# Optimization experiments

Measured on AMD Instinct MI355X. Metric: run time of the kernel, lower is better.

The kernel has to match this reference:

```python
import jax, jax.numpy as jnp
import numpy as np

B, T, N, D = 32, 50, 100, 4
E = N * (N - 1)
N_IN, N_HID, N_OUT = T * D, 256, 4


def _mlp(x, w1, b1, w2, b2):
    # Linear -> ReLU -> (dropout=0) -> Linear
    return jax.nn.relu(x @ w1 + b1) @ w2 + b2


def setup_inputs() -> dict:
    key = jax.random.key(0)
    ks = jax.random.split(key, 12)
    # fully-connected directed graph, no self loops
    idx = np.array([(i, j) for i in range(N) for j in range(N) if i != j], dtype=np.int64)
    recv, sendr = idx[:, 0], idx[:, 1]
    rec = jnp.asarray(np.eye(N, dtype=np.float32)[recv])    # [E, N]
    send = jnp.asarray(np.eye(N, dtype=np.float32)[sendr])  # [E, N]

    def lin(k, fan_in, fan_out):
        kw, kb = jax.random.split(k)
        w = jax.random.normal(kw, (fan_in, fan_out), jnp.float32) * 0.02
        b = jax.random.normal(kb, (fan_out,), jnp.float32) * 0.02
        return w, b

    x = jax.random.normal(ks[0], (B, T, N, D), jnp.float32)
    w1a, b1a = lin(ks[1], N_IN, N_HID)
    w1b, b1b = lin(ks[2], N_HID, N_HID)
    w2a, b2a = lin(ks[3], 2 * N_HID, N_HID)
    w2b, b2b = lin(ks[4], N_HID, N_HID)
    w3a, b3a = lin(ks[5], N_HID, N_HID)
    w3b, b3b = lin(ks[6], N_HID, N_HID)
    w4a, b4a = lin(ks[7], 3 * N_HID, N_HID)
    w4b, b4b = lin(ks[8], N_HID, N_HID)
    wo, bo = lin(ks[9], N_HID, N_OUT)
    return {"x": x, "rec": rec, "send": send,
            "w1a": w1a, "b1a": b1a, "w1b": w1b, "b1b": b1b,
            "w2a": w2a, "b2a": b2a, "w2b": w2b, "b2b": b2b,
            "w3a": w3a, "b3a": b3a, "w3b": w3b, "b3b": b3b,
            "w4a": w4a, "b4a": b4a, "w4b": w4b, "b4b": b4b,
            "wo": wo, "bo": bo}


def reference(x, rec, send,
              w1a, b1a, w1b, b1b,
              w2a, b2a, w2b, b2b,
              w3a, b3a, w3b, b3b,
              w4a, b4a, w4b, b4b,
              wo, bo):
    # [B, T, N, D] -> [B, N, T*D]
    h = jnp.transpose(x, (0, 2, 1, 3)).reshape(x.shape[0], x.shape[2], -1)
    h = _mlp(h, w1a, b1a, w1b, b1b)                       # [B, N, H]
    # v2e: gather receiver/sender node states to edges
    e = jnp.concatenate([jnp.einsum('en,bnh->beh', rec, h),
                         jnp.einsum('en,bnh->beh', send, h)], axis=2)  # [B, E, 2H]
    e = _mlp(e, w2a, b2a, w2b, b2b)                       # [B, E, H]
    x_skip = e
    # e2v: scatter edges back to nodes, normalize by n_nodes
    v = jnp.einsum('en,beh->bnh', rec, e) / e.shape[-2] * (e.shape[-2] / rec.shape[1])
    v = jnp.einsum('en,beh->bnh', rec, e) / rec.shape[1]  # incoming / incoming.size(1)=N
    v = _mlp(v, w3a, b3a, w3b, b3b)                       # [B, N, H]
    e2 = jnp.concatenate([jnp.einsum('en,bnh->beh', rec, v),
                          jnp.einsum('en,bnh->beh', send, v)], axis=2)  # [B, E, 2H]
    e2 = jnp.concatenate([e2, x_skip], axis=2)            # [B, E, 3H]
    e2 = _mlp(e2, w4a, b4a, w4b, b4b)                     # [B, E, H]
    return e2 @ wo + bo                                   # [B, E, n_out]
```

## Files before the change

kernel.cpp:

```cpp
#include <hip/hip_runtime.h>
#include <hip/hip_bf16.h>
#include <stdint.h>


typedef __attribute__((ext_vector_type(8))) short short8;
typedef __attribute__((ext_vector_type(4))) float float4v;
typedef __attribute__((ext_vector_type(4))) unsigned short ushort4v;
typedef __attribute__((ext_vector_type(4))) unsigned int uint4v;

__device__ inline float bf2f(unsigned short u) {
    union { unsigned int i; float f; } v; v.i = ((unsigned int)u) << 16; return v.f;
}

#if __has_builtin(__builtin_amdgcn_cvt_pk_bf16_f32)
typedef __attribute__((ext_vector_type(2))) __bf16 bf16x2;
__device__ inline unsigned int f2bf_pk(float a, float b) {
    union { bf16x2 v; unsigned int u; } c;
    c.v = __builtin_amdgcn_cvt_pk_bf16_f32(a, b);
    return c.u;
}
__device__ inline unsigned short f2bf(float f) {
    return (unsigned short)(f2bf_pk(f, f) & 0xFFFFu);
}
#else
__device__ inline unsigned short f2bf(float f) {
    union { float f; unsigned int i; } v; v.f = f;
    unsigned int i = v.i;
    return (unsigned short)((i + 0x7FFFu + ((i >> 16) & 1u)) >> 16);
}
__device__ inline unsigned int f2bf_pk(float a, float b) {
    return (unsigned int)f2bf(a) | ((unsigned int)f2bf(b) << 16);
}
#endif

__global__ __launch_bounds__(256) void prep_kernel(
        const float* __restrict__ x,
        const float* __restrict__ w1a, const float* __restrict__ w1b,
        const float* __restrict__ w2a, const float* __restrict__ w2b,
        const float* __restrict__ w3a, const float* __restrict__ w3b,
        const float* __restrict__ w4a, const float* __restrict__ b4a,
        const float* __restrict__ w4b, const float* __restrict__ b4b,
        const float* __restrict__ wo,  const float* __restrict__ bo,
        const float* __restrict__ b2b,
        unsigned short* __restrict__ Wp1a, unsigned short* __restrict__ Wp1b,
        unsigned short* __restrict__ Wp2r, unsigned short* __restrict__ Wp2s,
        unsigned short* __restrict__ Wp2b, unsigned short* __restrict__ Wp3a,
        unsigned short* __restrict__ Wp3b, unsigned short* __restrict__ Wp4r,
        unsigned short* __restrict__ Wp4s, unsigned short* __restrict__ Wpz,
        unsigned short* __restrict__ Wfp, float* __restrict__ bfv,
        float* __restrict__ b4ap, float* __restrict__ b2bs,
        unsigned short* __restrict__ hin) {
    int bx = blockIdx.x;
    int tid = threadIdx.x;
    if (bx < 2272) {
        const float* W; unsigned short* Wp; int Kin; int b0;
        if      (bx <  224) { W = w1a;             Wp = Wp1a; Kin = 200; b0 = 0;    }
        else if (bx <  480) { W = w1b;             Wp = Wp1b; Kin = 256; b0 = 224;  }
        else if (bx <  736) { W = w2a;             Wp = Wp2r; Kin = 256; b0 = 480;  }
        else if (bx <  992) { W = w2a + 256 * 256; Wp = Wp2s; Kin = 256; b0 = 736;  }
        else if (bx < 1248) { W = w2b;             Wp = Wp2b; Kin = 256; b0 = 992;  }
        else if (bx < 1504) { W = w3a;             Wp = Wp3a; Kin = 256; b0 = 1248; }
        else if (bx < 1760) { W = w3b;             Wp = Wp3b; Kin = 256; b0 = 1504; }
        else if (bx < 2016) { W = w4a;             Wp = Wp4r; Kin = 256; b0 = 1760; }
        else                { W = w4a + 256 * 256; Wp = Wp4s; Kin = 256; b0 = 2016; }
        int idx = (bx - b0) * 256 + tid;
        int k = idx >> 8, n = idx & 255;
        unsigned short v = (k < Kin) ? f2bf(W[k * 256 + n]) : (unsigned short)0;
        Wp[((size_t)(k >> 5) * 256 + n) * 32 + (k & 31)] = v;
    } else if (bx < 2528) {
        int k = bx - 2272, c = tid;
        float s = 0.f;
        for (int t = 0; t < 256; ++t)
            s += w2b[k * 256 + t] * w4a[(size_t)(512 + t) * 256 + c];
        int n = (c & ~31) + (c & 1) * 16 + ((c & 31) >> 1);
        Wpz[((size_t)(k >> 5) * 256 + n) * 32 + (k & 31)] = f2bf(s);
    } else if (bx < 2530) {
        int k = tid;
        if (bx == 2528) {
            float a[4] = {0.f, 0.f, 0.f, 0.f};
            for (int c = 0; c < 256; ++c) {
                float wv = w4b[k * 256 + c];
                #pragma unroll
                for (int o = 0; o < 4; ++o) a[o] += wv * wo[c * 4 + o];
            }
            #pragma unroll
            for (int n = 0; n < 16; ++n)
                Wfp[(size_t)(k >> 5) * 512 + n * 32 + (k & 31)] =
                    (n < 4) ? f2bf(a[n]) : (unsigned short)0;
            if (k < 4) {
                float s = bo[k];
                for (int c = 0; c < 256; ++c) s += b4b[c] * wo[c * 4 + k];
                bfv[k] = s;
            }
        } else {
            float s = b4a[k];
            for (int t = 0; t < 256; ++t)
                s += b2b[t] * w4a[(size_t)(512 + t) * 256 + k];
            b4ap[k] = s;
            b2bs[k] = 0.99f * b2b[k];
        }
    } else {
        int idx = (bx - 2530) * 256 + tid;
        if (idx < 3200 * 224) {
            int row = idx / 224;
            int c = idx - row * 224;
            int b = row / 100, n = row - b * 100;
            unsigned short v = 0;
            if (c < 200) {
                int t = c >> 2, d = c & 3;
                v = f2bf(x[(((size_t)(b * 50 + t)) * 100 + n) * 4 + d]);
            }
            hin[(size_t)row * 224 + c] = v;
        }
    }
}

__global__ __launch_bounds__(512) void node_fusedA_kernel(
        const unsigned short* __restrict__ hin,
        const unsigned short* __restrict__ Wp1a, const float* __restrict__ b1a,
        const unsigned short* __restrict__ Wp1b, const float* __restrict__ b1b,
        const unsigned short* __restrict__ Wp2r, const float* __restrict__ b2a,
        const unsigned short* __restrict__ Wp2s,
        unsigned short* __restrict__ U, unsigned short* __restrict__ Hs) {
    __shared__ __align__(16) unsigned short t1s[16 * 264];
    __shared__ __align__(16) unsigned short hs2[16 * 264];
    const int m0 = blockIdx.x * 16;
    const int tid  = threadIdx.x;
    const int wave = tid >> 6;
    const int lane = tid & 63;
    const int l15  = lane & 15;
    const int quad = lane >> 4;
    const int n0   = wave * 32;
    const int koff = quad * 8;

    {
        float4v acc[2];
        acc[0] = (float4v)(0.0f); acc[1] = (float4v)(0.0f);
        for (int kb = 0; kb < 7; ++kb) {
            short8 af = *(const short8*)(hin + (size_t)(m0 + l15) * 224 + kb * 32 + koff);
            #pragma unroll
            for (int ni = 0; ni < 2; ++ni) {
                short8 bf = *(const short8*)(Wp1a + ((size_t)kb * 256 + n0 + ni * 16 + l15) * 32 + koff);
                acc[ni] = __builtin_amdgcn_mfma_f32_16x16x32_bf16(af, bf, acc[ni], 0, 0, 0);
            }
        }
        #pragma unroll
        for (int ni = 0; ni < 2; ++ni) {
            int col = n0 + ni * 16 + l15;
            float bv = b1a[col];
            #pragma unroll
            for (int r = 0; r < 4; ++r) {
                float v = acc[ni][r] + bv;
                v = v > 0.f ? v : 0.f;
                t1s[(quad * 4 + r) * 264 + col] = f2bf(v);
            }
        }
    }
    __syncthreads();

    {
        float4v acc[2];
        acc[0] = (float4v)(0.0f); acc[1] = (float4v)(0.0f);
        for (int kb = 0; kb < 8; ++kb) {
            short8 af = *(const short8*)(&t1s[l15 * 264 + kb * 32 + koff]);
            #pragma unroll
            for (int ni = 0; ni < 2; ++ni) {
                short8 bf = *(const short8*)(Wp1b + ((size_t)kb * 256 + n0 + ni * 16 + l15) * 32 + koff);
                acc[ni] = __builtin_amdgcn_mfma_f32_16x16x32_bf16(af, bf, acc[ni], 0, 0, 0);
            }
        }
        #pragma unroll
        for (int ni = 0; ni < 2; ++ni) {
            int col = n0 + ni * 16 + l15;
            float bv = b1b[col];
            #pragma unroll
            for (int r = 0; r < 4; ++r)
                hs2[(quad * 4 + r) * 264 + col] = f2bf(acc[ni][r] + bv);
        }
    }
    __syncthreads();

    {
        float4v aU[2], aH[2];
        aU[0] = (float4v)(0.0f); aU[1] = (float4v)(0.0f);
        aH[0] = (float4v)(0.0f); aH[1] = (float4v)(0.0f);
        for (int kb = 0; kb < 8; ++kb) {
            short8 af = *(const short8*)(&hs2[l15 * 264 + kb * 32 + koff]);
            #pragma unroll
            for (int ni = 0; ni < 2; ++ni) {
                short8 bu = *(const short8*)(Wp2r + ((size_t)kb * 256 + n0 + ni * 16 + l15) * 32 + koff);
                short8 bh = *(const short8*)(Wp2s + ((size_t)kb * 256 + n0 + ni * 16 + l15) * 32 + koff);
                aU[ni] = __builtin_amdgcn_mfma_f32_16x16x32_bf16(af, bu, aU[ni], 0, 0, 0);
                aH[ni] = __builtin_amdgcn_mfma_f32_16x16x32_bf16(af, bh, aH[ni], 0, 0, 0);
            }
        }
        #pragma unroll
        for (int ni = 0; ni < 2; ++ni) {
            int col = n0 + ni * 16 + l15;
            float bv = b2a[col];
            #pragma unroll
            for (int r = 0; r < 4; ++r) {
                size_t o = (size_t)(m0 + quad * 4 + r) * 256 + col;
                U[o]  = f2bf(aU[ni][r] + bv);
                Hs[o] = f2bf(aH[ni][r]);
            }
        }
    }
}

__global__ __launch_bounds__(512) void node_fusedC_kernel(
        const unsigned short* __restrict__ U, const unsigned short* __restrict__ Hs,
        const unsigned short* __restrict__ Wp2b, const float* __restrict__ b2bs,
        const unsigned short* __restrict__ Wp3a, const float* __restrict__ b3a,
        const unsigned short* __restrict__ Wp3b, const float* __restrict__ b3b,
        const unsigned short* __restrict__ Wp4r, const float* __restrict__ b4ap,
        const unsigned short* __restrict__ Wp4s,
        unsigned short* __restrict__ C4, unsigned short* __restrict__ Vs) {
    __shared__ __align__(16) unsigned short buf0[16 * 264];
    __shared__ __align__(16) unsigned short buf1[16 * 264];
    const int m0 = blockIdx.x * 16;
    const int tid  = threadIdx.x;
    const int wave = tid >> 6;
    const int lane = tid & 63;
    const int l15  = lane & 15;
    const int quad = lane >> 4;
    const int n0   = wave * 32;
    const int koff = quad * 8;

    {
        const int rl = tid >> 5;
        const int ct = (tid & 31) * 8;
        const int g = m0 + rl;
        const int b = g / 100, i = g - b * 100;
        float u[8], s[8];
        {
            ushort4v u0 = *(const ushort4v*)(U + (size_t)g * 256 + ct);
            ushort4v u1 = *(const ushort4v*)(U + (size_t)g * 256 + ct + 4);
            #pragma unroll
            for (int e = 0; e < 4; ++e) { u[e] = bf2f(u0[e]); u[4 + e] = bf2f(u1[e]); }
            #pragma unroll
            for (int e = 0; e < 8; ++e) s[e] = 0.f;
        }
        const unsigned short* base = Hs + (size_t)b * 100 * 256 + ct;
        #pragma unroll 5
        for (int j = 0; j < 100; ++j) {
            ushort4v h0 = *(const ushort4v*)(base + (size_t)j * 256);
            ushort4v h1 = *(const ushort4v*)(base + (size_t)j * 256 + 4);
            #pragma unroll
            for (int e = 0; e < 4; ++e) {
                float v0 = u[e] + bf2f(h0[e]);     s[e]     += (v0 > 0.f ? v0 : 0.f);
                float v1 = u[4 + e] + bf2f(h1[e]); s[4 + e] += (v1 > 0.f ? v1 : 0.f);
            }
        }
        {
            ushort4v h0 = *(const ushort4v*)(base + (size_t)i * 256);
            ushort4v h1 = *(const ushort4v*)(base + (size_t)i * 256 + 4);
            #pragma unroll
            for (int e = 0; e < 4; ++e) {
                float v0 = u[e] + bf2f(h0[e]);     s[e]     -= (v0 > 0.f ? v0 : 0.f);
                float v1 = u[4 + e] + bf2f(h1[e]); s[4 + e] -= (v1 > 0.f ? v1 : 0.f);
            }
        }
        uint4v d;
        d[0] = f2bf_pk(s[0] * 0.01f, s[1] * 0.01f);
        d[1] = f2bf_pk(s[2] * 0.01f, s[3] * 0.01f);
        d[2] = f2bf_pk(s[4] * 0.01f, s[5] * 0.01f);
        d[3] = f2bf_pk(s[6] * 0.01f, s[7] * 0.01f);
        *(uint4v*)(&buf1[rl * 264 + ct]) = d;
    }
    __syncthreads();

    {
        float4v acc[2];
        acc[0] = (float4v)(0.0f); acc[1] = (float4v)(0.0f);
        for (int kb = 0; kb < 8; ++kb) {
            short8 af = *(const short8*)(&buf1[l15 * 264 + kb * 32 + koff]);
            #pragma unroll
            for (int ni = 0; ni < 2; ++ni) {
                short8 bf = *(const short8*)(Wp2b + ((size_t)kb * 256 + n0 + ni * 16 + l15) * 32 + koff);
                acc[ni] = __builtin_amdgcn_mfma_f32_16x16x32_bf16(af, bf, acc[ni], 0, 0, 0);
            }
        }
        #pragma unroll
        for (int ni = 0; ni < 2; ++ni) {
            int col = n0 + ni * 16 + l15;
            float bv = b2bs[col];
            #pragma unroll
            for (int r = 0; r < 4; ++r)
                buf0[(quad * 4 + r) * 264 + col] = f2bf(acc[ni][r] + bv);
        }
    }
    __syncthreads();

    {
        float4v acc[2];
        acc[0] = (float4v)(0.0f); acc[1] = (float4v)(0.0f);
        for (int kb = 0; kb < 8; ++kb) {
            short8 af = *(const short8*)(&buf0[l15 * 264 + kb * 32 + koff]);
            #pragma unroll
            for (int ni = 0; ni < 2; ++ni) {
                short8 bf = *(const short8*)(Wp3a + ((size_t)kb * 256 + n0 + ni * 16 + l15) * 32 + koff);
                acc[ni] = __builtin_amdgcn_mfma_f32_16x16x32_bf16(af, bf, acc[ni], 0, 0, 0);
            }
        }
        __syncthreads();
        #pragma unroll
        for (int ni = 0; ni < 2; ++ni) {
            int col = n0 + ni * 16 + l15;
            float bv = b3a[col];
            #pragma unroll
            for (int r = 0; r < 4; ++r) {
                float v = acc[ni][r] + bv;
                v = v > 0.f ? v : 0.f;
                buf1[(quad * 4 + r) * 264 + col] = f2bf(v);
            }
        }
    }
    __syncthreads();

    {
        float4v acc[2];
        acc[0] = (float4v)(0.0f); acc[1] = (float4v)(0.0f);
        for (int kb = 0; kb < 8; ++kb) {
            short8 af = *(const short8*)(&buf1[l15 * 264 + kb * 32 + koff]);
            #pragma unroll
            for (int ni = 0; ni < 2; ++ni) {
                short8 bf = *(const short8*)(Wp3b + ((size_t)kb * 256 + n0 + ni * 16 + l15) * 32 + koff);
                acc[ni] = __builtin_amdgcn_mfma_f32_16x16x32_bf16(af, bf, acc[ni], 0, 0, 0);
            }
        }
        __syncthreads();
        #pragma unroll
        for (int ni = 0; ni < 2; ++ni) {
            int col = n0 + ni * 16 + l15;
            float bv = b3b[col];
            #pragma unroll
            for (int r = 0; r < 4; ++r)
                buf0[(quad * 4 + r) * 264 + col] = f2bf(acc[ni][r] + bv);
        }
    }
    __syncthreads();

    {
        float4v aC[2], aV[2];
        aC[0] = (float4v)(0.0f); aC[1] = (float4v)(0.0f);
        aV[0] = (float4v)(0.0f); aV[1] = (float4v)(0.0f);
        for (int kb = 0; kb < 8; ++kb) {
            short8 af = *(const short8*)(&buf0[l15 * 264 + kb * 32 + koff]);
            #pragma unroll
            for (int ni = 0; ni < 2; ++ni) {
                short8 bc = *(const short8*)(Wp4r + ((size_t)kb * 256 + n0 + ni * 16 + l15) * 32 + koff);
                short8 bv = *(const short8*)(Wp4s + ((size_t)kb * 256 + n0 + ni * 16 + l15) * 32 + koff);
                aC[ni] = __builtin_amdgcn_mfma_f32_16x16x32_bf16(af, bc, aC[ni], 0, 0, 0);
                aV[ni] = __builtin_amdgcn_mfma_f32_16x16x32_bf16(af, bv, aV[ni], 0, 0, 0);
            }
        }
        #pragma unroll
        for (int ni = 0; ni < 2; ++ni) {
            int col = n0 + ni * 16 + l15;
            float bv = b4ap[col];
            #pragma unroll
            for (int r = 0; r < 4; ++r) {
                size_t o = (size_t)(m0 + quad * 4 + r) * 256 + col;
                C4[o] = f2bf(aC[ni][r] + bv);
                Vs[o] = f2bf(aV[ni][r]);
            }
        }
    }
}

__global__ __launch_bounds__(512, 6) void edge_phaseB_kernel(
        const unsigned short* __restrict__ Hs, const unsigned short* __restrict__ Vs,
        const unsigned short* __restrict__ U, const unsigned short* __restrict__ C4,
        const unsigned short* __restrict__ Wpz, const unsigned short* __restrict__ Wfp,
        const float* __restrict__ bfv,
        float* __restrict__ out) {
    __shared__ __align__(16) unsigned short t2s[64 * 264];
    __shared__ int jtab[64];
    const int g = blockIdx.x, hb = blockIdx.y;
    const int b = g / 100, nr = g - b * 100;
    const int nrows = hb ? 49 : 50;
    const int k0 = hb * 50;
    const int tid  = threadIdx.x;
    const int wave = tid >> 6;
    const int lane = tid & 63;
    const int l15  = lane & 15;
    const int quad = lane >> 4;
    const int n0   = wave * 32;
    const int koff = quad * 8;

    {
        const int c = lane * 4;
        ushort4v uv = *(const ushort4v*)(U + (size_t)g * 256 + c);
        float u0 = bf2f(uv[0]), u1 = bf2f(uv[1]), u2 = bf2f(uv[2]), u3 = bf2f(uv[3]);
        for (int r = wave; r < 64; r += 8) {
            int k = k0 + r;
            int j = (r < nrows) ? (k + (k >= nr ? 1 : 0)) : 0;
            if (lane == 0) jtab[r] = b * 100 + j;
            unsigned int p01 = 0, p23 = 0;
            if (r < nrows) {
                ushort4v hv = *(const ushort4v*)(Hs + (size_t)(b * 100 + j) * 256 + c);
                float t0 = u0 + bf2f(hv[0]); t0 = t0 > 0.f ? t0 : 0.f;
                float t1 = u1 + bf2f(hv[1]); t1 = t1 > 0.f ? t1 : 0.f;
                float t2 = u2 + bf2f(hv[2]); t2 = t2 > 0.f ? t2 : 0.f;
                float t3 = u3 + bf2f(hv[3]); t3 = t3 > 0.f ? t3 : 0.f;
                p01 = f2bf_pk(t0, t1);
                p23 = f2bf_pk(t2, t3);
            }
            unsigned int* dst = (unsigned int*)(&t2s[r * 264 + c]);
            dst[0] = p01;
            dst[1] = p23;
        }
    }
    __syncthreads();

    const int cp = n0 + 2 * l15;
    unsigned int c4p = *(const unsigned int*)(C4 + (size_t)g * 256 + cp);
    unsigned int vsp[16];
    #pragma unroll
    for (int mi = 0; mi < 4; ++mi)
        #pragma unroll
        for (int r = 0; r < 4; ++r)
            vsp[mi * 4 + r] = *(const unsigned int*)(Vs + (size_t)jtab[mi * 16 + quad * 4 + r] * 256 + cp);

    float c4v0 = bf2f((unsigned short)c4p);
    float c4v1 = bf2f((unsigned short)(c4p >> 16));
    float4v acc[4][2];
    #pragma unroll
    for (int mi = 0; mi < 4; ++mi) {
        acc[mi][0] = (float4v)(c4v0);
        acc[mi][1] = (float4v)(c4v1);
    }

    #pragma unroll 2
    for (int kb = 0; kb < 8; ++kb) {
        short8 bf0 = *(const short8*)(Wpz + ((size_t)kb * 256 + n0 + l15) * 32 + koff);
        short8 bf1 = *(const short8*)(Wpz + ((size_t)kb * 256 + n0 + 16 + l15) * 32 + koff);
        #pragma unroll
        for (int mi = 0; mi < 4; ++mi) {
            short8 af = *(const short8*)(&t2s[(mi * 16 + l15) * 264 + kb * 32 + koff]);
            acc[mi][0] = __builtin_amdgcn_mfma_f32_16x16x32_bf16(af, bf0, acc[mi][0], 0, 0, 0);
            acc[mi][1] = __builtin_amdgcn_mfma_f32_16x16x32_bf16(af, bf1, acc[mi][1], 0, 0, 0);
        }
    }
    __syncthreads();

    #pragma unroll
    for (int mi = 0; mi < 4; ++mi) {
        #pragma unroll
        for (int r = 0; r < 4; ++r) {
            int row = mi * 16 + quad * 4 + r;
            unsigned int vp = vsp[mi * 4 + r];
            float z0 = bf2f((unsigned short)vp) + acc[mi][0][r];
            float z1 = bf2f((unsigned short)(vp >> 16)) + acc[mi][1][r];
            z0 = z0 > 0.f ? z0 : 0.f;
            z1 = z1 > 0.f ? z1 : 0.f;
            *(unsigned int*)(&t2s[row * 264 + cp]) = f2bf_pk(z0, z1);
        }
    }
    __syncthreads();

    if (wave < 4) {
        float4v pacc = (float4v)(0.0f);
        #pragma unroll
        for (int kb = 0; kb < 8; ++kb) {
            short8 za = *(const short8*)(&t2s[(wave * 16 + l15) * 264 + kb * 32 + koff]);
            short8 wb = *(const short8*)(Wfp + (size_t)kb * 512 + l15 * 32 + koff);
            pacc = __builtin_amdgcn_mfma_f32_16x16x32_bf16(za, wb, pacc, 0, 0, 0);
        }
        if (l15 < 4) {
            float bv = bfv[l15];
            #pragma unroll
            for (int r = 0; r < 4; ++r) {
                int row = wave * 16 + quad * 4 + r;
                if (row < nrows)
                    out[((size_t)b * 9900 + nr * 99 + k0 + row) * 4 + l15] = pacc[r] + bv;
            }
        }
    }
}

extern "C" void kernel_launch(void* const* d_in, const int* in_sizes, int n_in,
                              void* d_out, int out_size, void* d_ws, size_t ws_size,
                              hipStream_t stream) {
    const float* x   = (const float*)d_in[0];
    const float* w1a = (const float*)d_in[3];
    const float* b1a = (const float*)d_in[4];
    const float* w1b = (const float*)d_in[5];
    const float* b1b = (const float*)d_in[6];
    const float* w2a = (const float*)d_in[7];
    const float* b2a = (const float*)d_in[8];
    const float* w2b = (const float*)d_in[9];
    const float* b2b = (const float*)d_in[10];
    const float* w3a = (const float*)d_in[11];
    const float* b3a = (const float*)d_in[12];
    const float* w3b = (const float*)d_in[13];
    const float* b3b = (const float*)d_in[14];
    const float* w4a = (const float*)d_in[15];
    const float* b4a = (const float*)d_in[16];
    const float* w4b = (const float*)d_in[17];
    const float* b4b = (const float*)d_in[18];
    const float* wo  = (const float*)d_in[19];
    const float* bo  = (const float*)d_in[20];
    float* out = (float*)d_out;
    (void)in_sizes; (void)n_in; (void)out_size; (void)ws_size;

    char* ws = (char*)d_ws;
    size_t off = 0;
    auto alloc = [&](size_t bytes) {
        size_t o = off;
        off = (off + bytes + 255) & ~(size_t)255;
        return o;
    };
    const size_t SLOT_BF = (size_t)3200 * 256 * 2;
    unsigned short* S_U  = (unsigned short*)(ws + alloc(SLOT_BF));
    unsigned short* S_Hs = (unsigned short*)(ws + alloc(SLOT_BF));
    unsigned short* S_Vs = (unsigned short*)(ws + alloc(SLOT_BF));
    unsigned short* S_4  = (unsigned short*)(ws + alloc(SLOT_BF));
    unsigned short* Wp1a = (unsigned short*)(ws + alloc(224 * 256 * 2));
    unsigned short* Wp1b = (unsigned short*)(ws + alloc(256 * 256 * 2));
    unsigned short* Wp2r = (unsigned short*)(ws + alloc(256 * 256 * 2));
    unsigned short* Wp2s = (unsigned short*)(ws + alloc(256 * 256 * 2));
    unsigned short* Wp2b = (unsigned short*)(ws + alloc(256 * 256 * 2));
    unsigned short* Wp3a = (unsigned short*)(ws + alloc(256 * 256 * 2));
    unsigned short* Wp3b = (unsigned short*)(ws + alloc(256 * 256 * 2));
    unsigned short* Wp4r = (unsigned short*)(ws + alloc(256 * 256 * 2));
    unsigned short* Wp4s = (unsigned short*)(ws + alloc(256 * 256 * 2));
    unsigned short* Wpz  = (unsigned short*)(ws + alloc(256 * 256 * 2));
    unsigned short* Wfp  = (unsigned short*)(ws + alloc(8 * 16 * 32 * 2));
    float*          bfv  = (float*)(ws + alloc(4 * 4));
    float*          b4ap = (float*)(ws + alloc(256 * 4));
    float*          b2bs = (float*)(ws + alloc(256 * 4));

    unsigned short* hin = S_4;
    unsigned short* C4  = S_4;

    hipLaunchKernelGGL(prep_kernel, dim3(5330), dim3(256), 0, stream,
                       x, w1a, w1b, w2a, w2b, w3a, w3b, w4a, b4a, w4b, b4b, wo, bo, b2b,
                       Wp1a, Wp1b, Wp2r, Wp2s, Wp2b, Wp3a, Wp3b, Wp4r, Wp4s, Wpz,
                       Wfp, bfv, b4ap, b2bs, hin);
    hipLaunchKernelGGL(node_fusedA_kernel, dim3(200), dim3(512), 0, stream,
                       hin, Wp1a, b1a, Wp1b, b1b, Wp2r, b2a, Wp2s, S_U, S_Hs);
    hipLaunchKernelGGL(node_fusedC_kernel, dim3(200), dim3(512), 0, stream,
                       S_U, S_Hs, Wp2b, b2bs, Wp3a, b3a, Wp3b, b3b, Wp4r, b4ap, Wp4s, C4, S_Vs);
    hipLaunchKernelGGL(edge_phaseB_kernel, dim3(3200, 2), dim3(512), 0, stream,
                       S_Hs, S_Vs, S_U, C4, Wpz, Wfp, bfv, out);
}
```

Before: 249.8 us.

## Pack edge tiles densely to 64 edges per block across receiver boundaries

The edge kernel previously used one block per (batch, receiver, half), which filled only 49-50 of the 64 MFMA rows and launched 6400 blocks. It now tiles the flattened edge list per batch into full 64-row blocks (155x32 grid), with each block spanning up to two receivers. Both receivers' U and C4 rows are selected per row. This removes wasted MFMA rows and about 22% of the blocks, at the cost of extra per-row selects and a second set of loads.

```diff
diff --git a/kernel.cpp b/kernel.cpp
--- a/kernel.cpp
+++ b/kernel.cpp
@@ -377,10 +377,12 @@
         float* __restrict__ out) {
     __shared__ __align__(16) unsigned short t2s[64 * 264];
     __shared__ int jtab[64];
-    const int g = blockIdx.x, hb = blockIdx.y;
-    const int b = g / 100, nr = g - b * 100;
-    const int nrows = hb ? 49 : 50;
-    const int k0 = hb * 50;
+    const int e0 = blockIdx.x * 64;
+    const int b  = blockIdx.y;
+    const int nE = (9900 - e0) < 64 ? (9900 - e0) : 64;
+    const int nr0 = e0 / 99;
+    const int nr1 = (nr0 < 99) ? nr0 + 1 : 99;
+    const int br  = (nr0 + 1) * 99 - e0;
     const int tid  = threadIdx.x;
     const int wave = tid >> 6;
     const int lane = tid & 63;
@@ -391,19 +393,25 @@
 
     {
         const int c = lane * 4;
-        ushort4v uv = *(const ushort4v*)(U + (size_t)g * 256 + c);
-        float u0 = bf2f(uv[0]), u1 = bf2f(uv[1]), u2 = bf2f(uv[2]), u3 = bf2f(uv[3]);
+        ushort4v uva = *(const ushort4v*)(U + (size_t)(b * 100 + nr0) * 256 + c);
+        ushort4v uvb = *(const ushort4v*)(U + (size_t)(b * 100 + nr1) * 256 + c);
+        float ua0 = bf2f(uva[0]), ua1 = bf2f(uva[1]), ua2 = bf2f(uva[2]), ua3 = bf2f(uva[3]);
+        float ub0 = bf2f(uvb[0]), ub1 = bf2f(uvb[1]), ub2 = bf2f(uvb[2]), ub3 = bf2f(uvb[3]);
         for (int r = wave; r < 64; r += 8) {
-            int k = k0 + r;
-            int j = (r < nrows) ? (k + (k >= nr ? 1 : 0)) : 0;
+            int sec = (r >= br) ? 1 : 0;
+            int nr  = sec ? nr1 : nr0;
+            int k   = e0 + r - nr * 99;
+            int j   = k + (k >= nr ? 1 : 0);
+            int valid = r < nE;
+            if (!valid) j = 0;
             if (lane == 0) jtab[r] = b * 100 + j;
             unsigned int p01 = 0, p23 = 0;
-            if (r < nrows) {
+            if (valid) {
                 ushort4v hv = *(const ushort4v*)(Hs + (size_t)(b * 100 + j) * 256 + c);
-                float t0 = u0 + bf2f(hv[0]); t0 = t0 > 0.f ? t0 : 0.f;
-                float t1 = u1 + bf2f(hv[1]); t1 = t1 > 0.f ? t1 : 0.f;
-                float t2 = u2 + bf2f(hv[2]); t2 = t2 > 0.f ? t2 : 0.f;
-                float t3 = u3 + bf2f(hv[3]); t3 = t3 > 0.f ? t3 : 0.f;
+                float t0 = (sec ? ub0 : ua0) + bf2f(hv[0]); t0 = t0 > 0.f ? t0 : 0.f;
+                float t1 = (sec ? ub1 : ua1) + bf2f(hv[1]); t1 = t1 > 0.f ? t1 : 0.f;
+                float t2 = (sec ? ub2 : ua2) + bf2f(hv[2]); t2 = t2 > 0.f ? t2 : 0.f;
+                float t3 = (sec ? ub3 : ua3) + bf2f(hv[3]); t3 = t3 > 0.f ? t3 : 0.f;
                 p01 = f2bf_pk(t0, t1);
                 p23 = f2bf_pk(t2, t3);
             }
@@ -415,7 +423,8 @@
     __syncthreads();
 
     const int cp = n0 + 2 * l15;
-    unsigned int c4p = *(const unsigned int*)(C4 + (size_t)g * 256 + cp);
+    unsigned int c4a = *(const unsigned int*)(C4 + (size_t)(b * 100 + nr0) * 256 + cp);
+    unsigned int c4b = *(const unsigned int*)(C4 + (size_t)(b * 100 + nr1) * 256 + cp);
     unsigned int vsp[16];
     #pragma unroll
     for (int mi = 0; mi < 4; ++mi)
@@ -423,13 +432,11 @@
         for (int r = 0; r < 4; ++r)
             vsp[mi * 4 + r] = *(const unsigned int*)(Vs + (size_t)jtab[mi * 16 + quad * 4 + r] * 256 + cp);
 
-    float c4v0 = bf2f((unsigned short)c4p);
-    float c4v1 = bf2f((unsigned short)(c4p >> 16));
     float4v acc[4][2];
     #pragma unroll
     for (int mi = 0; mi < 4; ++mi) {
-        acc[mi][0] = (float4v)(c4v0);
-        acc[mi][1] = (float4v)(c4v1);
+        acc[mi][0] = (float4v)(0.0f);
+        acc[mi][1] = (float4v)(0.0f);
     }
 
     #pragma unroll 2
@@ -451,8 +458,9 @@
         for (int r = 0; r < 4; ++r) {
             int row = mi * 16 + quad * 4 + r;
             unsigned int vp = vsp[mi * 4 + r];
-            float z0 = bf2f((unsigned short)vp) + acc[mi][0][r];
-            float z1 = bf2f((unsigned short)(vp >> 16)) + acc[mi][1][r];
+            unsigned int cw = (row >= br) ? c4b : c4a;
+            float z0 = bf2f((unsigned short)vp) + bf2f((unsigned short)cw) + acc[mi][0][r];
+            float z1 = bf2f((unsigned short)(vp >> 16)) + bf2f((unsigned short)(cw >> 16)) + acc[mi][1][r];
             z0 = z0 > 0.f ? z0 : 0.f;
             z1 = z1 > 0.f ? z1 : 0.f;
             *(unsigned int*)(&t2s[row * 264 + cp]) = f2bf_pk(z0, z1);
@@ -473,8 +481,8 @@
             #pragma unroll
             for (int r = 0; r < 4; ++r) {
                 int row = wave * 16 + quad * 4 + r;
-                if (row < nrows)
-                    out[((size_t)b * 9900 + nr * 99 + k0 + row) * 4 + l15] = pacc[r] + bv;
+                if (row < nE)
+                    out[((size_t)b * 9900 + e0 + row) * 4 + l15] = pacc[r] + bv;
             }
         }
     }
@@ -543,6 +551,6 @@
                        hin, Wp1a, b1a, Wp1b, b1b, Wp2r, b2a, Wp2s, S_U, S_Hs);
     hipLaunchKernelGGL(node_fusedC_kernel, dim3(200), dim3(512), 0, stream,
                        S_U, S_Hs, Wp2b, b2bs, Wp3a, b3a, Wp3b, b3b, Wp4r, b4ap, Wp4s, C4, S_Vs);
-    hipLaunchKernelGGL(edge_phaseB_kernel, dim3(3200, 2), dim3(512), 0, stream,
+    hipLaunchKernelGGL(edge_phaseB_kernel, dim3(155, 32), dim3(512), 0, stream,
                        S_Hs, S_Vs, S_U, C4, Wpz, Wfp, bfv, out);
 }
```

New measurement: 238.5 us. 4.5% less time.
